# Performance work log

Hardware: AMD Instinct MI355X
Metric: run time of the kernel (lower is better)

The kernel has to match this reference:

```python
import jax, jax.numpy as jnp
import numpy as np

B, I, O, G = 4096, 256, 256, 32


def setup_inputs() -> dict:
    key = jax.random.key(0)
    k1, k2, k3, k4 = jax.random.split(key, 4)
    x = jax.random.normal(k1, (B, I), dtype=jnp.float32)
    fouriercoeffs = jax.random.normal(k2, (2, O, I, G), dtype=jnp.float32) / (np.sqrt(I) * np.sqrt(G))
    bias = jnp.zeros((1, O), dtype=jnp.float32)
    mask = jnp.ones((I, O), dtype=jnp.float32)
    # scale_base = mu/sqrt(I) + sigma*(rand*2-1)/sqrt(I), mu=0, sigma=1
    scale_base = (jax.random.uniform(k3, (I, O), dtype=jnp.float32) * 2.0 - 1.0) / np.sqrt(I)
    scale_fft = jnp.ones((I, O), dtype=jnp.float32) * (1.0 / np.sqrt(I)) * mask
    return {"x": x, "fouriercoeffs": fouriercoeffs, "bias": bias, "mask": mask,
            "scale_base": scale_base, "scale_fft": scale_fft}


def reference(x, fouriercoeffs, bias, mask, scale_base, scale_fft):
    gridsize = fouriercoeffs.shape[-1]
    k = jnp.arange(1, gridsize + 1, dtype=x.dtype)          # (G,)
    kx = x[:, :, None] * k                                   # (B, I, G)
    c = jnp.cos(kx)
    s = jnp.sin(kx)
    # einsum 'dbik,djik->bij' with d=2 split into cos/sin parts
    y = jnp.einsum('bik,jik->bij', c, fouriercoeffs[0]) \
        + jnp.einsum('bik,jik->bij', s, fouriercoeffs[1])    # (B, I, O)
    base = jax.nn.silu(x)                                     # SiLU base branch
    y = scale_base[None, :, :] * base[:, :, None] + scale_fft[None, :, :] * y
    y = (mask[None, :, :] * y).sum(axis=1)                    # sum over inputdim -> (B, O)
    y = y + bias
    return y
```

## Files before the change

kernel.cpp:

```cpp
#include <hip/hip_runtime.h>
#include <stdint.h>


#define I_DIM 256
#define O_DIM 256
#define G_DIM 32
#define B_DIM 4096

#define BM 128
#define BN 128
#define KSPLIT 16
#define ICH 16
#define PITCH 72

typedef short s8v __attribute__((ext_vector_type(8)));
typedef float f4v __attribute__((ext_vector_type(4)));

__device__ __forceinline__ uint32_t pack2bf16(float a, float b) {
  uint32_t ua = __builtin_bit_cast(uint32_t, a);
  uint32_t ub = __builtin_bit_cast(uint32_t, b);
  ua += 0x7FFFu + ((ua >> 16) & 1u);
  ub += 0x7FFFu + ((ub >> 16) & 1u);
  return (ua >> 16) | (ub & 0xFFFF0000u);
}
__device__ __forceinline__ unsigned short bf16_rne(float a) {
  uint32_t ua = __builtin_bit_cast(uint32_t, a);
  ua += 0x7FFFu + ((ua >> 16) & 1u);
  return (unsigned short)(ua >> 16);
}
__device__ __forceinline__ uint32_t pack2bf16_f(float a, float b) {
  uint32_t ua = __builtin_bit_cast(uint32_t, a) + 0x8000u;
  uint32_t ub = __builtin_bit_cast(uint32_t, b) + 0x8000u;
  return (ua >> 16) | (ub & 0xFFFF0000u);
}
__device__ __forceinline__ float silu_f(float v) { return v / (1.0f + __expf(-v)); }

__device__ __forceinline__ void gen_feat(float xv, int half, uint32_t* fb) {
  float s, c;
  __sincosf(xv, &s, &c);
  const float m2 = 2.f * c;
  float f0 = half ? s : c;
  float f1 = m2 * f0 - (half ? 0.f : 1.f);
  fb[0] = pack2bf16_f(f0, f1);
  #pragma unroll
  for (int p = 1; p < 16; ++p) {
    float f2 = m2 * f1 - f0;
    float f3 = m2 * f2 - f1;
    fb[p] = pack2bf16_f(f2, f3);
    f0 = f2; f1 = f3;
  }
}

__global__ __launch_bounds__(256) void prep_bs_kernel(
    const float* __restrict__ fc, const float* __restrict__ mask,
    const float* __restrict__ sfft, short* __restrict__ Bp)
{
  const int gid = blockIdx.x * 256 + threadIdx.x;
  const int h = gid & 1;
  const int d = (gid >> 1) & 1;
  const int p = gid >> 2;
  const int i = p >> 8, j = p & 255;
  const size_t ij = (size_t)i * O_DIM + j;
  const float sf = sfft[ij] * mask[ij];
  const float* src = fc + (size_t)d * (O_DIM * I_DIM * G_DIM)
                        + ((size_t)j * I_DIM + i) * G_DIM + h * 16;
  uint32_t w[8];
  #pragma unroll
  for (int q = 0; q < 4; ++q) {
    float4 v = ((const float4*)src)[q];
    w[2*q]   = pack2bf16(v.x * sf, v.y * sf);
    w[2*q+1] = pack2bf16(v.z * sf, v.w * sf);
  }
  uint4* dst = (uint4*)(Bp + (size_t)p * 64);
  const int xr = j & 7;
  #pragma unroll
  for (int c = 0; c < 2; ++c)
    dst[(4 * d + 2 * h + c) ^ xr] = make_uint4(w[4*c], w[4*c+1], w[4*c+2], w[4*c+3]);
}

__global__ __launch_bounds__(256, 4) void kan_main2(
    const float* __restrict__ x,
    const short* __restrict__ Bp,
    const float* __restrict__ mask,
    const float* __restrict__ scale_base,
    unsigned short* __restrict__ partial)
{
  __shared__ short A_lds[BM * 64];
  __shared__ short B_lds[BN * 64];

  const int tid = threadIdx.x;
  const int bx  = blockIdx.x;
  const int kc  = bx & 15;
  const int bn  = (bx >> 4) & 1;
  const int bm  = bx >> 5;
  const int i0  = kc * ICH;

  const int lane = tid & 63;
  const int wave = tid >> 6;
  const int wm   = wave & 1;
  const int wn   = wave >> 1;
  const int l15  = lane & 15;
  const int quad = lane >> 4;

  f4v acc[4][4];
  #pragma unroll
  for (int a = 0; a < 4; ++a)
    #pragma unroll
    for (int b = 0; b < 4; ++b)
      acc[a][b] = (f4v){0.f, 0.f, 0.f, 0.f};

  const int row  = tid >> 1;
  const int half = tid & 1;
  const int mg   = bm * BM + row;
  const int jg   = bn * BN + row;
  const int xr   = row & 7;

  const float* xrow = x + (size_t)mg * I_DIM + i0;
  uint4* Arow = (uint4*)&A_lds[row * 64];
  const int c0 = half * 4;
  const int q0 = wave * 4;
  const size_t dma_lane_off = (size_t)lane * 8;

  uint32_t aNext[16];
  gen_feat(xrow[0], half, aNext);

  for (int it = 0; it < ICH; ++it) {
    __syncthreads();

    Arow[(c0 + 0) ^ xr] = make_uint4(aNext[0],  aNext[1],  aNext[2],  aNext[3]);
    Arow[(c0 + 1) ^ xr] = make_uint4(aNext[4],  aNext[5],  aNext[6],  aNext[7]);
    Arow[(c0 + 2) ^ xr] = make_uint4(aNext[8],  aNext[9],  aNext[10], aNext[11]);
    Arow[(c0 + 3) ^ xr] = make_uint4(aNext[12], aNext[13], aNext[14], aNext[15]);

    {
      const size_t rbase = ((size_t)(i0 + it) * 256 + bn * BN) * 64;
      #pragma unroll
      for (int c = 0; c < 4; ++c) {
        const int q = q0 + c;
        const short* g = Bp + rbase + (size_t)q * 8 * 64 + dma_lane_off;
        __builtin_amdgcn_global_load_lds(
            (const __attribute__((address_space(1))) void*)g,
            (__attribute__((address_space(3))) void*)&B_lds[q * 8 * 64],
            16, 0, 0);
      }
    }

    __syncthreads();

    if (it + 1 < ICH) gen_feat(xrow[it + 1], half, aNext);

    #pragma unroll
    for (int ks = 0; ks < 2; ++ks) {
      s8v a[4], b[4];
      #pragma unroll
      for (int tm = 0; tm < 4; ++tm) {
        const int r = wm * 64 + tm * 16 + l15;
        a[tm] = *(const s8v*)&A_lds[r * 64 + (((ks * 4 + quad) ^ (r & 7)) * 8)];
      }
      #pragma unroll
      for (int tn = 0; tn < 4; ++tn) {
        const int r = wn * 64 + tn * 16 + l15;
        b[tn] = *(const s8v*)&B_lds[r * 64 + (((ks * 4 + quad) ^ (r & 7)) * 8)];
      }
      #pragma unroll
      for (int tm = 0; tm < 4; ++tm)
        #pragma unroll
        for (int tn = 0; tn < 4; ++tn)
          acc[tm][tn] = __builtin_amdgcn_mfma_f32_16x16x32_bf16(a[tm], b[tn], acc[tm][tn], 0, 0, 0);
    }
  }

  __syncthreads();
  {
    const float* xb = xrow + half * 8;
    float4 v0 = ((const float4*)xb)[0];
    float4 v1 = ((const float4*)xb)[1];
    uint32_t a0 = pack2bf16(silu_f(v0.x), silu_f(v0.y));
    uint32_t a1 = pack2bf16(silu_f(v0.z), silu_f(v0.w));
    uint32_t a2 = pack2bf16(silu_f(v1.x), silu_f(v1.y));
    uint32_t a3 = pack2bf16(silu_f(v1.z), silu_f(v1.w));
    Arow[half ^ xr]       = make_uint4(a0, a1, a2, a3);
    Arow[(2 + half) ^ xr] = make_uint4(0, 0, 0, 0);

    uint32_t w[4];
    #pragma unroll
    for (int p = 0; p < 4; ++p) {
      const int ia = i0 + half * 8 + 2 * p;
      const size_t o0 = (size_t)ia * O_DIM + jg;
      const size_t o1 = o0 + O_DIM;
      w[p] = pack2bf16(scale_base[o0] * mask[o0], scale_base[o1] * mask[o1]);
    }
    uint4* Brow = (uint4*)&B_lds[row * 64];
    Brow[half ^ xr]       = make_uint4(w[0], w[1], w[2], w[3]);
    Brow[(2 + half) ^ xr] = make_uint4(0, 0, 0, 0);
  }
  __syncthreads();
  {
    s8v a[4], b[4];
    #pragma unroll
    for (int tm = 0; tm < 4; ++tm) {
      const int r = wm * 64 + tm * 16 + l15;
      a[tm] = *(const s8v*)&A_lds[r * 64 + ((quad ^ (r & 7)) * 8)];
    }
    #pragma unroll
    for (int tn = 0; tn < 4; ++tn) {
      const int r = wn * 64 + tn * 16 + l15;
      b[tn] = *(const s8v*)&B_lds[r * 64 + ((quad ^ (r & 7)) * 8)];
    }
    #pragma unroll
    for (int tm = 0; tm < 4; ++tm)
      #pragma unroll
      for (int tn = 0; tn < 4; ++tn)
        acc[tm][tn] = __builtin_amdgcn_mfma_f32_16x16x32_bf16(a[tm], b[tn], acc[tm][tn], 0, 0, 0);
  }

  unsigned short* pbase = partial + (size_t)kc * B_DIM * O_DIM;
  #pragma unroll
  for (int tm = 0; tm < 4; ++tm) {
    #pragma unroll
    for (int tn = 0; tn < 4; ++tn) {
      const int n_g = bn * BN + wn * 64 + tn * 16 + l15;
      f4v v = acc[tm][tn];
      #pragma unroll
      for (int r = 0; r < 4; ++r) {
        const int m_g = bm * BM + wm * 64 + tm * 16 + quad * 4 + r;
        pbase[(size_t)m_g * O_DIM + n_g] = bf16_rne(v[r]);
      }
    }
  }
}

__global__ __launch_bounds__(256) void reduce_kernel(
    const unsigned short* __restrict__ partial, const float* __restrict__ bias,
    float* __restrict__ out)
{
  const int g  = blockIdx.x * 256 + threadIdx.x;
  const int m  = g >> 5;
  const int n8 = (g & 31) << 3;
  const unsigned short* p = partial + (size_t)m * O_DIM + n8;

  float acc[8];
  {
    float4 b0 = ((const float4*)(bias + n8))[0];
    float4 b1 = ((const float4*)(bias + n8))[1];
    acc[0] = b0.x; acc[1] = b0.y; acc[2] = b0.z; acc[3] = b0.w;
    acc[4] = b1.x; acc[5] = b1.y; acc[6] = b1.z; acc[7] = b1.w;
  }
  #pragma unroll
  for (int kc = 0; kc < KSPLIT; ++kc) {
    const uint4 v = *(const uint4*)(p + (size_t)kc * (B_DIM * O_DIM));
    acc[0] += __builtin_bit_cast(float, v.x << 16);
    acc[1] += __builtin_bit_cast(float, v.x & 0xFFFF0000u);
    acc[2] += __builtin_bit_cast(float, v.y << 16);
    acc[3] += __builtin_bit_cast(float, v.y & 0xFFFF0000u);
    acc[4] += __builtin_bit_cast(float, v.z << 16);
    acc[5] += __builtin_bit_cast(float, v.z & 0xFFFF0000u);
    acc[6] += __builtin_bit_cast(float, v.w << 16);
    acc[7] += __builtin_bit_cast(float, v.w & 0xFFFF0000u);
  }
  float* o = out + (size_t)m * O_DIM + n8;
  ((float4*)o)[0] = make_float4(acc[0], acc[1], acc[2], acc[3]);
  ((float4*)o)[1] = make_float4(acc[4], acc[5], acc[6], acc[7]);
}

__global__ __launch_bounds__(256, 4) void kan_fft_fallback(
    const float* __restrict__ x, const float* __restrict__ fc,
    const float* __restrict__ bias, const float* __restrict__ mask,
    const float* __restrict__ scale_base, const float* __restrict__ scale_fft,
    float* __restrict__ out)
{
  __shared__ short A_lds[BM * PITCH];
  __shared__ short B_lds[BN * PITCH];

  const int tid = threadIdx.x;
  const int bx  = blockIdx.x;
  const int kc  = bx & 15;
  const int bn  = (bx >> 4) & 1;
  const int bm  = bx >> 5;
  const int i0  = kc * ICH;

  const int lane = tid & 63;
  const int wave = tid >> 6;
  const int wm   = wave & 1;
  const int wn   = wave >> 1;
  const int l15  = lane & 15;
  const int kgrp = (lane >> 4) * 8;

  f4v acc[4][4];
  #pragma unroll
  for (int a = 0; a < 4; ++a)
    #pragma unroll
    for (int b = 0; b < 4; ++b)
      acc[a][b] = (f4v){0.f, 0.f, 0.f, 0.f};

  const int row  = tid >> 1;
  const int half = tid & 1;
  const int mg   = bm * BM + row;
  const int jg   = bn * BN + row;

  const float* xrow   = x + (size_t)mg * I_DIM + i0;
  const float* fcbase = fc + (size_t)half * (O_DIM * I_DIM * G_DIM)
                           + ((size_t)jg * I_DIM + i0) * G_DIM;
  uint32_t* Arow = (uint32_t*)&A_lds[row * PITCH + half * 32];
  uint32_t* Brow = (uint32_t*)&B_lds[row * PITCH + half * 32];

  for (int it = 0; it < ICH; ++it) {
    __syncthreads();
    {
      uint32_t fb[16];
      gen_feat(xrow[it], half, fb);
      ((uint4*)Arow)[0] = make_uint4(fb[0],  fb[1],  fb[2],  fb[3]);
      ((uint4*)Arow)[1] = make_uint4(fb[4],  fb[5],  fb[6],  fb[7]);
      ((uint4*)Arow)[2] = make_uint4(fb[8],  fb[9],  fb[10], fb[11]);
      ((uint4*)Arow)[3] = make_uint4(fb[12], fb[13], fb[14], fb[15]);
    }
    {
      const int i = i0 + it;
      const size_t ij = (size_t)i * O_DIM + jg;
      const float sf  = scale_fft[ij] * mask[ij];
      const float* src = fcbase + it * G_DIM;
      uint32_t wb[16];
      #pragma unroll
      for (int q = 0; q < 8; ++q) {
        float4 v = ((const float4*)src)[q];
        wb[2*q]   = pack2bf16(v.x * sf, v.y * sf);
        wb[2*q+1] = pack2bf16(v.z * sf, v.w * sf);
      }
      ((uint4*)Brow)[0] = make_uint4(wb[0],  wb[1],  wb[2],  wb[3]);
      ((uint4*)Brow)[1] = make_uint4(wb[4],  wb[5],  wb[6],  wb[7]);
      ((uint4*)Brow)[2] = make_uint4(wb[8],  wb[9],  wb[10], wb[11]);
      ((uint4*)Brow)[3] = make_uint4(wb[12], wb[13], wb[14], wb[15]);
    }
    __syncthreads();
    #pragma unroll
    for (int ks = 0; ks < 2; ++ks) {
      s8v a[4], b[4];
      #pragma unroll
      for (int tm = 0; tm < 4; ++tm)
        a[tm] = *(const s8v*)&A_lds[(wm * 64 + tm * 16 + l15) * PITCH + ks * 32 + kgrp];
      #pragma unroll
      for (int tn = 0; tn < 4; ++tn)
        b[tn] = *(const s8v*)&B_lds[(wn * 64 + tn * 16 + l15) * PITCH + ks * 32 + kgrp];
      #pragma unroll
      for (int tm = 0; tm < 4; ++tm)
        #pragma unroll
        for (int tn = 0; tn < 4; ++tn)
          acc[tm][tn] = __builtin_amdgcn_mfma_f32_16x16x32_bf16(a[tm], b[tn], acc[tm][tn], 0, 0, 0);
    }
  }

  __syncthreads();
  {
    const float* xb = xrow + half * 8;
    float4 v0 = ((const float4*)xb)[0];
    float4 v1 = ((const float4*)xb)[1];
    uint32_t a0 = pack2bf16(silu_f(v0.x), silu_f(v0.y));
    uint32_t a1 = pack2bf16(silu_f(v0.z), silu_f(v0.w));
    uint32_t a2 = pack2bf16(silu_f(v1.x), silu_f(v1.y));
    uint32_t a3 = pack2bf16(silu_f(v1.z), silu_f(v1.w));
    ((uint4*)&A_lds[row * PITCH + half * 8])[0]      = make_uint4(a0, a1, a2, a3);
    ((uint4*)&A_lds[row * PITCH + 16 + half * 8])[0] = make_uint4(0, 0, 0, 0);
    uint32_t w[4];
    #pragma unroll
    for (int p = 0; p < 4; ++p) {
      const int ia = i0 + half * 8 + 2 * p;
      const size_t o0 = (size_t)ia * O_DIM + jg;
      const size_t o1 = o0 + O_DIM;
      w[p] = pack2bf16(scale_base[o0] * mask[o0], scale_base[o1] * mask[o1]);
    }
    ((uint4*)&B_lds[row * PITCH + half * 8])[0]      = make_uint4(w[0], w[1], w[2], w[3]);
    ((uint4*)&B_lds[row * PITCH + 16 + half * 8])[0] = make_uint4(0, 0, 0, 0);
  }
  __syncthreads();
  {
    s8v a[4], b[4];
    #pragma unroll
    for (int tm = 0; tm < 4; ++tm)
      a[tm] = *(const s8v*)&A_lds[(wm * 64 + tm * 16 + l15) * PITCH + kgrp];
    #pragma unroll
    for (int tn = 0; tn < 4; ++tn)
      b[tn] = *(const s8v*)&B_lds[(wn * 64 + tn * 16 + l15) * PITCH + kgrp];
    #pragma unroll
    for (int tm = 0; tm < 4; ++tm)
      #pragma unroll
      for (int tn = 0; tn < 4; ++tn)
        acc[tm][tn] = __builtin_amdgcn_mfma_f32_16x16x32_bf16(a[tm], b[tn], acc[tm][tn], 0, 0, 0);
  }

  const int quad = lane >> 4;
  #pragma unroll
  for (int tm = 0; tm < 4; ++tm) {
    #pragma unroll
    for (int tn = 0; tn < 4; ++tn) {
      const int n_g = bn * BN + wn * 64 + tn * 16 + l15;
      f4v v = acc[tm][tn];
      #pragma unroll
      for (int r = 0; r < 4; ++r) {
        const int m_g = bm * BM + wm * 64 + tm * 16 + quad * 4 + r;
        float val = v[r];
        if (kc == 0) val += bias[n_g];
        atomicAdd(&out[(size_t)m_g * O_DIM + n_g], val);
      }
    }
  }
}

extern "C" void kernel_launch(void* const* d_in, const int* in_sizes, int n_in,
                              void* d_out, int out_size, void* d_ws, size_t ws_size,
                              hipStream_t stream) {
  const float* x          = (const float*)d_in[0];
  const float* fc         = (const float*)d_in[1];
  const float* bias       = (const float*)d_in[2];
  const float* mask       = (const float*)d_in[3];
  const float* scale_base = (const float*)d_in[4];
  const float* scale_fft  = (const float*)d_in[5];
  float* out = (float*)d_out;

  const size_t BP_B    = (size_t)I_DIM * O_DIM * 64 * 2;
  const size_t PARTH_B = (size_t)KSPLIT * B_DIM * O_DIM * 2;

  if (ws_size >= BP_B + PARTH_B) {
    short*          Bp      = (short*)d_ws;
    unsigned short* partial = (unsigned short*)((char*)d_ws + BP_B);
    prep_bs_kernel<<<dim3(1024), dim3(256), 0, stream>>>(fc, mask, scale_fft, Bp);
    kan_main2<<<dim3(1024), dim3(256), 0, stream>>>(x, Bp, mask, scale_base, partial);
    reduce_kernel<<<dim3(512), dim3(256), 0, stream>>>(partial, bias, out);
  } else {
    hipMemsetAsync(d_out, 0, (size_t)out_size * sizeof(float), stream);
    kan_fft_fallback<<<dim3(1024), dim3(256), 0, stream>>>(
        x, fc, bias, mask, scale_base, scale_fft, out);
  }
}
```

Baseline: 128.7 us.

## Fuse prep, GEMM and reduce into one cooperative kernel with grid syncs

Replaces the three separate launches (weight prep, split-K MFMA GEMM, partial reduction) with a single cooperative kernel that uses grid-wide barriers between phases. Each block prepares the slice of packed bf16 weights for its own K-chunk, syncs the grid, runs the GEMM tile, syncs again, then reduces the partials. The aim is to remove the launch gaps and tail effects between kernels. In exchange it adds two grid barriers, requires all 1024 blocks to be co-resident at 4 blocks per CU, and keeps the old three-kernel path as a fallback if the cooperative launch fails.

```diff
diff --git a/kernel.cpp b/kernel.cpp
--- a/kernel.cpp
+++ b/kernel.cpp
@@ -1,5 +1,8 @@
 #include <hip/hip_runtime.h>
+#include <hip/hip_cooperative_groups.h>
 #include <stdint.h>
+
+namespace cg = cooperative_groups;
 
 
 #define I_DIM 256
@@ -50,6 +53,210 @@
     f0 = f2; f1 = f3;
   }
 }
+
+__global__ __launch_bounds__(256, 4) void kan_fused(
+    const float* __restrict__ x, const float* __restrict__ fc,
+    const float* __restrict__ bias, const float* __restrict__ mask,
+    const float* __restrict__ scale_base, const float* __restrict__ sfft,
+    short* __restrict__ Bp, unsigned short* __restrict__ partial,
+    float* __restrict__ out)
+{
+  __shared__ short A_lds[BM * 64];
+  __shared__ short B_lds[BN * 64];
+
+  const int tid = threadIdx.x;
+  const int bx  = blockIdx.x;
+  const int kc  = bx & 15;
+
+  {
+    const int g  = (bx >> 4) * 256 + tid;
+    const int h  = g & 1;
+    const int d  = (g >> 1) & 1;
+    const int pl = g >> 2;
+    const int j  = pl & 255;
+    const int i  = kc * ICH + (pl >> 8);
+    const int p  = i * 256 + j;
+    const size_t ij = (size_t)i * O_DIM + j;
+    const float sf = sfft[ij] * mask[ij];
+    const float* src = fc + (size_t)d * (O_DIM * I_DIM * G_DIM)
+                          + ((size_t)j * I_DIM + i) * G_DIM + h * 16;
+    uint32_t w[8];
+    #pragma unroll
+    for (int q = 0; q < 4; ++q) {
+      float4 v = ((const float4*)src)[q];
+      w[2*q]   = pack2bf16(v.x * sf, v.y * sf);
+      w[2*q+1] = pack2bf16(v.z * sf, v.w * sf);
+    }
+    uint4* dst = (uint4*)(Bp + (size_t)p * 64);
+    const int xr2 = j & 7;
+    #pragma unroll
+    for (int c = 0; c < 2; ++c)
+      dst[(4 * d + 2 * h + c) ^ xr2] = make_uint4(w[4*c], w[4*c+1], w[4*c+2], w[4*c+3]);
+  }
+
+  cg::this_grid().sync();
+
+  {
+    const int bn  = (bx >> 4) & 1;
+    const int bm  = bx >> 5;
+    const int i0  = kc * ICH;
+
+    const int lane = tid & 63;
+    const int wave = tid >> 6;
+    const int wm   = wave & 1;
+    const int wn   = wave >> 1;
+    const int l15  = lane & 15;
+    const int quad = lane >> 4;
+
+    f4v acc[4][4];
+    #pragma unroll
+    for (int a = 0; a < 4; ++a)
+      #pragma unroll
+      for (int b = 0; b < 4; ++b)
+        acc[a][b] = (f4v){0.f, 0.f, 0.f, 0.f};
+
+    const int row  = tid >> 1;
+    const int half = tid & 1;
+    const int mg   = bm * BM + row;
+    const int jg   = bn * BN + row;
+    const int xr   = row & 7;
+
+    const float* xrow = x + (size_t)mg * I_DIM + i0;
+    uint4* Arow = (uint4*)&A_lds[row * 64];
+    const int c0 = half * 4;
+    const int q0 = wave * 4;
+    const size_t dma_lane_off = (size_t)lane * 8;
+
+    uint32_t aNext[16];
+    gen_feat(xrow[0], half, aNext);
+
+    for (int it = 0; it < ICH; ++it) {
+      __syncthreads();
+
+      Arow[(c0 + 0) ^ xr] = make_uint4(aNext[0],  aNext[1],  aNext[2],  aNext[3]);
+      Arow[(c0 + 1) ^ xr] = make_uint4(aNext[4],  aNext[5],  aNext[6],  aNext[7]);
+      Arow[(c0 + 2) ^ xr] = make_uint4(aNext[8],  aNext[9],  aNext[10], aNext[11]);
+      Arow[(c0 + 3) ^ xr] = make_uint4(aNext[12], aNext[13], aNext[14], aNext[15]);
+
+      {
+        const size_t rbase = ((size_t)(i0 + it) * 256 + bn * BN) * 64;
+        #pragma unroll
+        for (int c = 0; c < 4; ++c) {
+          const int q = q0 + c;
+          const short* g = Bp + rbase + (size_t)q * 8 * 64 + dma_lane_off;
+          __builtin_amdgcn_global_load_lds(
+              (const __attribute__((address_space(1))) void*)g,
+              (__attribute__((address_space(3))) void*)&B_lds[q * 8 * 64],
+              16, 0, 0);
+        }
+      }
+
+      __syncthreads();
+
+      if (it + 1 < ICH) gen_feat(xrow[it + 1], half, aNext);
+
+      #pragma unroll
+      for (int ks = 0; ks < 2; ++ks) {
+        s8v a[4], b[4];
+        #pragma unroll
+        for (int tm = 0; tm < 4; ++tm) {
+          const int r = wm * 64 + tm * 16 + l15;
+          a[tm] = *(const s8v*)&A_lds[r * 64 + (((ks * 4 + quad) ^ (r & 7)) * 8)];
+        }
+        #pragma unroll
+        for (int tn = 0; tn < 4; ++tn) {
+          const int r = wn * 64 + tn * 16 + l15;
+          b[tn] = *(const s8v*)&B_lds[r * 64 + (((ks * 4 + quad) ^ (r & 7)) * 8)];
+        }
+        #pragma unroll
+        for (int tm = 0; tm < 4; ++tm)
+          #pragma unroll
+          for (int tn = 0; tn < 4; ++tn)
+            acc[tm][tn] = __builtin_amdgcn_mfma_f32_16x16x32_bf16(a[tm], b[tn], acc[tm][tn], 0, 0, 0);
+      }
+    }
+
+    __syncthreads();
+    {
+      const float* xb = xrow + half * 8;
+      float4 v0 = ((const float4*)xb)[0];
+      float4 v1 = ((const float4*)xb)[1];
+      uint32_t a0 = pack2bf16(silu_f(v0.x), silu_f(v0.y));
+      uint32_t a1 = pack2bf16(silu_f(v0.z), silu_f(v0.w));
+      uint32_t a2 = pack2bf16(silu_f(v1.x), silu_f(v1.y));
+      uint32_t a3 = pack2bf16(silu_f(v1.z), silu_f(v1.w));
+      Arow[half ^ xr]       = make_uint4(a0, a1, a2, a3);
+      Arow[(2 + half) ^ xr] = make_uint4(0, 0, 0, 0);
+
+      uint32_t w[4];
+      #pragma unroll
+      for (int p = 0; p < 4; ++p) {
+        const int ia = i0 + half * 8 + 2 * p;
+        const size_t o0 = (size_t)ia * O_DIM + jg;
+        const size_t o1 = o0 + O_DIM;
+        w[p] = pack2bf16(scale_base[o0] * mask[o0], scale_base[o1] * mask[o1]);
+      }
+      uint4* Brow = (uint4*)&B_lds[row * 64];
+      Brow[half ^ xr]       = make_uint4(w[0], w[1], w[2], w[3]);
+      Brow[(2 + half) ^ xr] = make_uint4(0, 0, 0, 0);
+    }
+    __syncthreads();
+    {
+      s8v a[4], b[4];
+      #pragma unroll
+      for (int tm = 0; tm < 4; ++tm) {
+        const int r = wm * 64 + tm * 16 + l15;
+        a[tm] = *(const s8v*)&A_lds[r * 64 + ((quad ^ (r & 7)) * 8)];
+      }
+      #pragma unroll
+      for (int tn = 0; tn < 4; ++tn) {
+        const int r = wn * 64 + tn * 16 + l15;
+        b[tn] = *(const s8v*)&B_lds[r * 64 + ((quad ^ (r & 7)) * 8)];
+      }
+      #pragma unroll
+      for (int tm = 0; tm < 4; ++tm)
+        #pragma unroll
+        for (int tn = 0; tn < 4; ++tn)
+          acc[tm][tn] = __builtin_amdgcn_mfma_f32_16x16x32_bf16(a[tm], b[tn], acc[tm][tn], 0, 0, 0);
+    }
+
+    unsigned short* pbase = partial + (size_t)kc * B_DIM * O_DIM;
+    #pragma unroll
+    for (int tm = 0; tm < 4; ++tm) {
+      #pragma unroll
+      for (int tn = 0; tn < 4; ++tn) {
+        const int n_g = bn * BN + wn * 64 + tn * 16 + l15;
+        f4v v = acc[tm][tn];
+        #pragma unroll
+        for (int r = 0; r < 4; ++r) {
+          const int m_g = bm * BM + wm * 64 + tm * 16 + quad * 4 + r;
+          pbase[(size_t)m_g * O_DIM + n_g] = bf16_rne(v[r]);
+        }
+      }
+    }
+  }
+
+  cg::this_grid().sync();
+
+  {
+    const int g  = bx * 256 + tid;
+    const int m  = g >> 6;
+    const int n4 = (g & 63) << 2;
+    const unsigned short* pp = partial + (size_t)m * O_DIM + n4;
+    float4 b4 = ((const float4*)(bias + n4))[0];
+    float a0 = b4.x, a1 = b4.y, a2 = b4.z, a3 = b4.w;
+    #pragma unroll
+    for (int k2 = 0; k2 < KSPLIT; ++k2) {
+      const uint2 v = *(const uint2*)(pp + (size_t)k2 * (B_DIM * O_DIM));
+      a0 += __builtin_bit_cast(float, v.x << 16);
+      a1 += __builtin_bit_cast(float, v.x & 0xFFFF0000u);
+      a2 += __builtin_bit_cast(float, v.y << 16);
+      a3 += __builtin_bit_cast(float, v.y & 0xFFFF0000u);
+    }
+    ((float4*)(out + (size_t)m * O_DIM + n4))[0] = make_float4(a0, a1, a2, a3);
+  }
+}
+
 
 __global__ __launch_bounds__(256) void prep_bs_kernel(
     const float* __restrict__ fc, const float* __restrict__ mask,
@@ -422,9 +629,18 @@
   if (ws_size >= BP_B + PARTH_B) {
     short*          Bp      = (short*)d_ws;
     unsigned short* partial = (unsigned short*)((char*)d_ws + BP_B);
-    prep_bs_kernel<<<dim3(1024), dim3(256), 0, stream>>>(fc, mask, scale_fft, Bp);
-    kan_main2<<<dim3(1024), dim3(256), 0, stream>>>(x, Bp, mask, scale_base, partial);
-    reduce_kernel<<<dim3(512), dim3(256), 0, stream>>>(partial, bias, out);
+
+    void* args[] = {(void*)&x, (void*)&fc, (void*)&bias, (void*)&mask,
+                    (void*)&scale_base, (void*)&scale_fft,
+                    (void*)&Bp, (void*)&partial, (void*)&out};
+    hipError_t e = hipLaunchCooperativeKernel((const void*)kan_fused,
+                                              dim3(1024), dim3(256),
+                                              args, 0, stream);
+    if (e != hipSuccess) {
+      prep_bs_kernel<<<dim3(1024), dim3(256), 0, stream>>>(fc, mask, scale_fft, Bp);
+      kan_main2<<<dim3(1024), dim3(256), 0, stream>>>(x, Bp, mask, scale_base, partial);
+      reduce_kernel<<<dim3(512), dim3(256), 0, stream>>>(partial, bias, out);
+    }
   } else {
     hipMemsetAsync(d_out, 0, (size_t)out_size * sizeof(float), stream);
     kan_fft_fallback<<<dim3(1024), dim3(256), 0, stream>>>(
```

Measured after the change: 379.5 us. 2.95x slower.

## Replace split-K partial buffer and reduce kernel with fp32 atomic accumulation

Applied to the files above, without the earlier changes.

The main GEMM kernel now adds its split-K results straight into the output with unsafe fp32 atomics. This removes the bf16 partial buffer (16 slices of B×O) and the separate reduce kernel. The prep kernel initialises the output with the bias so no memset is needed. The trade-off is 16-way atomic contention per output element, plus nondeterministic summation order, in exchange for avoiding a large write and read-back of partials and one launch.

```diff
diff --git a/kernel.cpp b/kernel.cpp
--- a/kernel.cpp
+++ b/kernel.cpp
@@ -22,11 +22,6 @@
   ua += 0x7FFFu + ((ua >> 16) & 1u);
   ub += 0x7FFFu + ((ub >> 16) & 1u);
   return (ua >> 16) | (ub & 0xFFFF0000u);
-}
-__device__ __forceinline__ unsigned short bf16_rne(float a) {
-  uint32_t ua = __builtin_bit_cast(uint32_t, a);
-  ua += 0x7FFFu + ((ua >> 16) & 1u);
-  return (unsigned short)(ua >> 16);
 }
 __device__ __forceinline__ uint32_t pack2bf16_f(float a, float b) {
   uint32_t ua = __builtin_bit_cast(uint32_t, a) + 0x8000u;
@@ -53,7 +48,8 @@
 
 __global__ __launch_bounds__(256) void prep_bs_kernel(
     const float* __restrict__ fc, const float* __restrict__ mask,
-    const float* __restrict__ sfft, short* __restrict__ Bp)
+    const float* __restrict__ sfft, const float* __restrict__ bias,
+    short* __restrict__ Bp, float* __restrict__ out)
 {
   const int gid = blockIdx.x * 256 + threadIdx.x;
   const int h = gid & 1;
@@ -76,14 +72,17 @@
   #pragma unroll
   for (int c = 0; c < 2; ++c)
     dst[(4 * d + 2 * h + c) ^ xr] = make_uint4(w[4*c], w[4*c+1], w[4*c+2], w[4*c+3]);
-}
-
-__global__ __launch_bounds__(256, 4) void kan_main2(
+
+  const int n4 = (gid & 63) << 2;
+  ((float4*)(out + (size_t)gid * 4))[0] = ((const float4*)(bias + n4))[0];
+}
+
+__global__ __launch_bounds__(256, 4) void kan_main3(
     const float* __restrict__ x,
     const short* __restrict__ Bp,
     const float* __restrict__ mask,
     const float* __restrict__ scale_base,
-    unsigned short* __restrict__ partial)
+    float* __restrict__ out)
 {
   __shared__ short A_lds[BM * 64];
   __shared__ short B_lds[BN * 64];
@@ -214,7 +213,6 @@
         acc[tm][tn] = __builtin_amdgcn_mfma_f32_16x16x32_bf16(a[tm], b[tn], acc[tm][tn], 0, 0, 0);
   }
 
-  unsigned short* pbase = partial + (size_t)kc * B_DIM * O_DIM;
   #pragma unroll
   for (int tm = 0; tm < 4; ++tm) {
     #pragma unroll
@@ -224,43 +222,10 @@
       #pragma unroll
       for (int r = 0; r < 4; ++r) {
         const int m_g = bm * BM + wm * 64 + tm * 16 + quad * 4 + r;
-        pbase[(size_t)m_g * O_DIM + n_g] = bf16_rne(v[r]);
-      }
-    }
-  }
-}
-
-__global__ __launch_bounds__(256) void reduce_kernel(
-    const unsigned short* __restrict__ partial, const float* __restrict__ bias,
-    float* __restrict__ out)
-{
-  const int g  = blockIdx.x * 256 + threadIdx.x;
-  const int m  = g >> 5;
-  const int n8 = (g & 31) << 3;
-  const unsigned short* p = partial + (size_t)m * O_DIM + n8;
-
-  float acc[8];
-  {
-    float4 b0 = ((const float4*)(bias + n8))[0];
-    float4 b1 = ((const float4*)(bias + n8))[1];
-    acc[0] = b0.x; acc[1] = b0.y; acc[2] = b0.z; acc[3] = b0.w;
-    acc[4] = b1.x; acc[5] = b1.y; acc[6] = b1.z; acc[7] = b1.w;
-  }
-  #pragma unroll
-  for (int kc = 0; kc < KSPLIT; ++kc) {
-    const uint4 v = *(const uint4*)(p + (size_t)kc * (B_DIM * O_DIM));
-    acc[0] += __builtin_bit_cast(float, v.x << 16);
-    acc[1] += __builtin_bit_cast(float, v.x & 0xFFFF0000u);
-    acc[2] += __builtin_bit_cast(float, v.y << 16);
-    acc[3] += __builtin_bit_cast(float, v.y & 0xFFFF0000u);
-    acc[4] += __builtin_bit_cast(float, v.z << 16);
-    acc[5] += __builtin_bit_cast(float, v.z & 0xFFFF0000u);
-    acc[6] += __builtin_bit_cast(float, v.w << 16);
-    acc[7] += __builtin_bit_cast(float, v.w & 0xFFFF0000u);
-  }
-  float* o = out + (size_t)m * O_DIM + n8;
-  ((float4*)o)[0] = make_float4(acc[0], acc[1], acc[2], acc[3]);
-  ((float4*)o)[1] = make_float4(acc[4], acc[5], acc[6], acc[7]);
+        unsafeAtomicAdd(&out[(size_t)m_g * O_DIM + n_g], v[r]);
+      }
+    }
+  }
 }
 
 __global__ __launch_bounds__(256, 4) void kan_fft_fallback(
@@ -416,15 +381,12 @@
   const float* scale_fft  = (const float*)d_in[5];
   float* out = (float*)d_out;
 
-  const size_t BP_B    = (size_t)I_DIM * O_DIM * 64 * 2;
-  const size_t PARTH_B = (size_t)KSPLIT * B_DIM * O_DIM * 2;
-
-  if (ws_size >= BP_B + PARTH_B) {
-    short*          Bp      = (short*)d_ws;
-    unsigned short* partial = (unsigned short*)((char*)d_ws + BP_B);
-    prep_bs_kernel<<<dim3(1024), dim3(256), 0, stream>>>(fc, mask, scale_fft, Bp);
-    kan_main2<<<dim3(1024), dim3(256), 0, stream>>>(x, Bp, mask, scale_base, partial);
-    reduce_kernel<<<dim3(512), dim3(256), 0, stream>>>(partial, bias, out);
+  const size_t BP_B = (size_t)I_DIM * O_DIM * 64 * 2;
+
+  if (ws_size >= BP_B) {
+    short* Bp = (short*)d_ws;
+    prep_bs_kernel<<<dim3(1024), dim3(256), 0, stream>>>(fc, mask, scale_fft, bias, Bp, out);
+    kan_main3<<<dim3(1024), dim3(256), 0, stream>>>(x, Bp, mask, scale_base, out);
   } else {
     hipMemsetAsync(d_out, 0, (size_t)out_size * sizeof(float), stream);
     kan_fft_fallback<<<dim3(1024), dim3(256), 0, stream>>>(
```

Result: slower. 156.2 us (+21.3%).
